# Optimization experiments

Measured on AMD Instinct MI355X. Metric: run time of the kernel, lower is better.

The kernel has to match this reference:

```python
import jax, jax.numpy as jnp
import numpy as np

B = 16384      # number of batched 6-node FC graphs
A = 6          # num_agents (nodes per graph)
D_OBS = 128    # raw observation dim
D_EMB = 250    # embedding / GAT feature dim
H = 3          # GAT heads (head outputs averaged to keep dim 250)
HID = 256
N_ACT = 5
NEG_SLOPE = 0.2


def setup_inputs() -> dict:
    key = jax.random.key(0)
    ks = jax.random.split(key, 16)
    def w(i, shape, scale=0.05):
        return jax.random.normal(ks[i], shape, dtype=jnp.float32) * scale
    return {
        "x": jax.random.normal(ks[0], (B * A, D_OBS), dtype=jnp.float32),
        "W_emb": w(1, (D_OBS, D_EMB)), "b_emb": jnp.zeros((D_EMB,), jnp.float32),
        "W_gat": w(2, (H, D_EMB, D_EMB)),
        "a_l": w(3, (H, D_EMB)), "a_r": w(4, (H, D_EMB)),
        "W1": w(5, (2 * D_EMB, HID)), "b1": jnp.zeros((HID,), jnp.float32),
        "W2": w(6, (HID, N_ACT)), "b2": jnp.zeros((N_ACT,), jnp.float32),
        "V1": w(7, (2 * D_EMB, HID)), "vb1": jnp.zeros((HID,), jnp.float32),
        "V2": w(8, (HID, 1)), "vb2": jnp.zeros((1,), jnp.float32),
    }


def reference(x, W_emb, b_emb, W_gat, a_l, a_r, W1, b1, W2, b2, V1, vb1, V2, vb2):
    # embedding layer
    h = jax.nn.relu(x @ W_emb + b_emb)                       # [N, 250]
    hb = h.reshape(B, A, D_EMB)                              # [B, 6, 250]
    # GAT on fully-connected 6-node graphs (incl. self edges), dense-masked form
    Wh = jnp.einsum("bad,hde->bhae", hb, W_gat)              # [B, H, 6, 250]
    el = jnp.einsum("bhae,he->bha", Wh, a_l)                 # dst term
    er = jnp.einsum("bhae,he->bha", Wh, a_r)                 # src term
    e = jax.nn.leaky_relu(el[:, :, :, None] + er[:, :, None, :], NEG_SLOPE)  # [B,H,6,6]
    attn = jax.nn.softmax(e, axis=-1)                        # edge softmax over neighbors
    gat = jnp.einsum("bhij,bhje->bhie", attn, Wh).mean(axis=1)  # mean over heads -> [B,6,250]
    feat = jnp.concatenate([hb, gat], axis=-1).reshape(B * A, 2 * D_EMB)  # [N, 500]
    # actor head (reg1)
    probs = jax.nn.softmax(jax.nn.relu(feat @ W1 + b1) @ W2 + b2, axis=-1)  # [N, 5]
    # critic head (reg2)
    value = jax.nn.relu(feat @ V1 + vb1) @ V2 + vb2           # [N, 1]
    return jnp.concatenate([probs, value], axis=-1)          # [N, 6]
```

## Files before the change

kernel.cpp:

```cpp
#include <hip/hip_runtime.h>

typedef unsigned short u16;
typedef unsigned int   u32;
typedef unsigned long long u64;
typedef __attribute__((ext_vector_type(4))) int   i32x4;
typedef __attribute__((ext_vector_type(4))) float f32x4;
typedef __attribute__((ext_vector_type(8))) short s16x8;

#define NROWS 98304L
#define LDF   512

__device__ __forceinline__ u16 f2bf(float x) {
  union { float f; u32 u; } v; v.f = x;
  return (u16)((v.u + 0x7FFFu + ((v.u >> 16) & 1u)) >> 16);
}
__device__ __forceinline__ float bf2f(u16 b) {
  union { float f; u32 u; } v; v.u = ((u32)b) << 16;
  return v.f;
}

__device__ __forceinline__ void gload_lds16(const u16* g, u16* l) {
  __builtin_amdgcn_global_load_lds(
      (const __attribute__((address_space(1))) unsigned int*)g,
      (__attribute__((address_space(3))) unsigned int*)l, 16, 0, 0);
}

__global__ __launch_bounds__(256)
void prep_weights(const float* __restrict__ W_emb, const float* __restrict__ b_emb,
                  const float* __restrict__ W_gat, const float* __restrict__ a_l,
                  const float* __restrict__ a_r, const float* __restrict__ W1,
                  const float* __restrict__ b1, const float* __restrict__ V1,
                  const float* __restrict__ vb1,
                  u16* __restrict__ Wemb_t, u16* __restrict__ Wgat_t,
                  u16* __restrict__ W1V1_t, float* __restrict__ bembp,
                  float* __restrict__ b1vb1)
{
  const int idx = blockIdx.x * 256 + threadIdx.x;
  const int stride = gridDim.x * 256;
  for (int t = idx; t < 256 * 128; t += stride) {
    int n = t >> 7, k = t & 127;
    Wemb_t[t] = f2bf(n < 250 ? W_emb[k * 250 + n] : 0.f);
  }
  for (int t = idx; t < 3 * 256 * 256; t += stride) {
    int h = t >> 16, rem = t & 65535, e = rem >> 8, d = rem & 255;
    float v = 0.f;
    if (e < 250 && d < 250) {
      v = W_gat[(h * 250 + d) * 250 + e];
    } else if ((e == 250 || e == 251) && d < 250) {
      const float* av = ((e == 250) ? a_l : a_r) + h * 250;
      const float* wrow = W_gat + ((long)h * 250 + d) * 250;
      float s = 0.f;
      for (int q = 0; q < 250; q++) s += wrow[q] * av[q];
      v = s;
    }
    Wgat_t[t] = f2bf(v);
  }
  for (int t = idx; t < 512 * 512; t += stride) {
    int n = t >> 9, k = t & 511;
    const float* src = (n < 256) ? W1 : V1;
    int col = n & 255;
    float v = 0.f;
    if (k < 250) v = src[k * 256 + col];
    else if (k >= 256 && k < 506) v = src[(k - 6) * 256 + col];
    W1V1_t[t] = f2bf(v);
  }
  for (int t = idx; t < 512; t += stride) b1vb1[t] = (t < 256) ? b1[t] : vb1[t - 256];
  for (int t = idx; t < 256; t += stride) bembp[t] = (t < 250) ? b_emb[t] : 0.f;
}

__global__ __launch_bounds__(256)
void cvt_x(const float* __restrict__ x, u16* __restrict__ xb)
{
  const long n = NROWS * 128;
  long i = ((long)blockIdx.x * 256 + threadIdx.x) * 8;
  const long stride = (long)gridDim.x * 256 * 8;
  for (; i < n; i += stride) {
    f32x4 a = *(const f32x4*)(x + i);
    f32x4 b = *(const f32x4*)(x + i + 4);
    i32x4 o;
    o[0] = (int)((u32)f2bf(a[0]) | ((u32)f2bf(a[1]) << 16));
    o[1] = (int)((u32)f2bf(a[2]) | ((u32)f2bf(a[3]) << 16));
    o[2] = (int)((u32)f2bf(b[0]) | ((u32)f2bf(b[1]) << 16));
    o[3] = (int)((u32)f2bf(b[2]) | ((u32)f2bf(b[3]) << 16));
    *(i32x4*)(xb + i) = o;
  }
}

template<int KSTEPS, int EPI>
__global__ __launch_bounds__(256, 2)
void gemm_bf16(const u16* __restrict__ A, int lda,
               const u16* __restrict__ B, int ldb, long strideB,
               u16* __restrict__ C, int ldc, long strideC,
               const float* __restrict__ bias, int nb)
{
  __shared__ __align__(16) u16 At[128 * 64];
  __shared__ __align__(16) u16 Bt[128 * 64];
  const int tid = threadIdx.x;
  const int w = tid >> 6, lane = tid & 63;
  const int fl = lane & 15, fh = lane >> 4;
  const int wr = (w >> 1) * 64, wc = (w & 1) * 64;
  const int srow = lane >> 3;
  const int scol = (((lane & 7) ^ srow) << 3);
  const int swz = (fl & 7) << 3;

  const int nidx = blockIdx.x % nb;
  const int zidx = blockIdx.x / nb;
  const int midx = blockIdx.y;

  const u16* Ab = A + (long)midx * 128 * lda;
  const u16* Bb = B + (long)zidx * strideB + (long)nidx * 128 * ldb;
  u16* Cb = C + (long)zidx * strideC + (long)midx * 128 * ldc + nidx * 128;
  const float* biasb = bias + nidx * 128;

  f32x4 acc[4][4];
  #pragma unroll
  for (int m = 0; m < 4; m++)
    #pragma unroll
    for (int n = 0; n < 4; n++)
      acc[m][n] = f32x4{0.f, 0.f, 0.f, 0.f};

  for (int ks = 0; ks < KSTEPS; ks++) {
    __syncthreads();
    #pragma unroll
    for (int c = 0; c < 4; c++) {
      const int row = w * 32 + c * 8 + srow;
      gload_lds16(Ab + (long)row * lda + ks * 64 + scol, At + (w * 4 + c) * 512);
      gload_lds16(Bb + (long)row * ldb + ks * 64 + scol, Bt + (w * 4 + c) * 512);
    }
    __syncthreads();
    #pragma unroll
    for (int kk = 0; kk < 2; kk++) {
      s16x8 af[4], bfr[4];
      #pragma unroll
      for (int m = 0; m < 4; m++)
        af[m] = *(const s16x8*)(At + (wr + m * 16 + fl) * 64 + ((kk * 32 + fh * 8) ^ swz));
      #pragma unroll
      for (int n = 0; n < 4; n++)
        bfr[n] = *(const s16x8*)(Bt + (wc + n * 16 + fl) * 64 + ((kk * 32 + fh * 8) ^ swz));
      #pragma unroll
      for (int m = 0; m < 4; m++)
        #pragma unroll
        for (int n = 0; n < 4; n++)
          acc[m][n] = __builtin_amdgcn_mfma_f32_16x16x32_bf16(af[m], bfr[n], acc[m][n], 0, 0, 0);
    }
  }
  #pragma unroll
  for (int m = 0; m < 4; m++) {
    const int r0 = wr + m * 16 + fh * 4;
    #pragma unroll
    for (int n = 0; n < 4; n++) {
      const int col = wc + n * 16 + fl;
      float bvv = 0.f;
      if constexpr (EPI == 1) bvv = biasb[col];
      f32x4 v = acc[m][n];
      #pragma unroll
      for (int r = 0; r < 4; r++) {
        float xv = v[r];
        if constexpr (EPI == 1) xv = fmaxf(xv + bvv, 0.f);
        Cb[(long)(r0 + r) * ldc + col] = f2bf(xv);
      }
    }
  }
}

__global__ __launch_bounds__(1024, 2)
void gemm3_heads(const u16* __restrict__ A,
                 const u16* __restrict__ B,
                 const float* __restrict__ b1vb1,
                 const float* __restrict__ W2,
                 const float* __restrict__ b2,
                 const float* __restrict__ V2,
                 const float* __restrict__ vb2,
                 float* __restrict__ out)
{
  __shared__ __align__(16) u16 At[128 * 64];
  __shared__ __align__(16) u16 Bt[512 * 64];
  __shared__ float pstage[8][128][6];
  const int tid = threadIdx.x;
  const int w = tid >> 6, lane = tid & 63;
  const int fl = lane & 15, fh = lane >> 4;
  const int wrow = w >> 3, wcol = w & 7;
  const int srow = lane >> 3;
  const int schunk = (((lane & 7) ^ srow) << 3);
  const int swz = (fl & 7) << 3;

  const u16* Ab = A + (long)blockIdx.x * 128 * 512;

  f32x4 acc[4][4];
  #pragma unroll
  for (int m = 0; m < 4; m++)
    #pragma unroll
    for (int n = 0; n < 4; n++)
      acc[m][n] = f32x4{0.f, 0.f, 0.f, 0.f};

  for (int ks = 0; ks < 8; ks++) {
    __syncthreads();
    gload_lds16(Ab + (long)(w * 8 + srow) * 512 + ks * 64 + schunk, At + w * 512);
    #pragma unroll
    for (int p = 0; p < 4; p++)
      gload_lds16(B + (long)(p * 128 + w * 8 + srow) * 512 + ks * 64 + schunk,
                  Bt + p * 8192 + w * 512);
    __syncthreads();
    #pragma unroll
    for (int kk = 0; kk < 2; kk++) {
      s16x8 af[4], bfr[4];
      #pragma unroll
      for (int m = 0; m < 4; m++)
        af[m] = *(const s16x8*)(At + (wrow * 64 + m * 16 + fl) * 64 + ((kk * 32 + fh * 8) ^ swz));
      #pragma unroll
      for (int n = 0; n < 4; n++)
        bfr[n] = *(const s16x8*)(Bt + (wcol * 64 + n * 16 + fl) * 64 + ((kk * 32 + fh * 8) ^ swz));
      #pragma unroll
      for (int m = 0; m < 4; m++)
        #pragma unroll
        for (int n = 0; n < 4; n++)
          acc[m][n] = __builtin_amdgcn_mfma_f32_16x16x32_bf16(af[m], bfr[n], acc[m][n], 0, 0, 0);
    }
  }

  float bv[4];
  #pragma unroll
  for (int n = 0; n < 4; n++) bv[n] = b1vb1[wcol * 64 + n * 16 + fl];

  if (wcol < 4) {
    #pragma unroll
    for (int m = 0; m < 4; m++) {
      float ps[4][5];
      #pragma unroll
      for (int r = 0; r < 4; r++)
        #pragma unroll
        for (int j = 0; j < 5; j++) ps[r][j] = 0.f;
      #pragma unroll
      for (int n = 0; n < 4; n++) {
        const int col = wcol * 64 + n * 16 + fl;
        const float* w2c = W2 + col * 5;
        float w2r[5];
        #pragma unroll
        for (int j = 0; j < 5; j++) w2r[j] = w2c[j];
        #pragma unroll
        for (int r = 0; r < 4; r++) {
          float hid = fmaxf(acc[m][n][r] + bv[n], 0.f);
          #pragma unroll
          for (int j = 0; j < 5; j++) ps[r][j] += hid * w2r[j];
        }
      }
      #pragma unroll
      for (int off = 1; off < 16; off <<= 1)
        #pragma unroll
        for (int r = 0; r < 4; r++)
          #pragma unroll
          for (int j = 0; j < 5; j++) ps[r][j] += __shfl_xor(ps[r][j], off, 16);
      if (fl == 0) {
        const int row = wrow * 64 + m * 16 + fh * 4;
        #pragma unroll
        for (int r = 0; r < 4; r++)
          #pragma unroll
          for (int j = 0; j < 5; j++) pstage[wcol][row + r][j] = ps[r][j];
      }
    }
  } else {
    #pragma unroll
    for (int m = 0; m < 4; m++) {
      float ps[4];
      #pragma unroll
      for (int r = 0; r < 4; r++) ps[r] = 0.f;
      #pragma unroll
      for (int n = 0; n < 4; n++) {
        const int col = wcol * 64 + n * 16 + fl;
        const float v2c = V2[col - 256];
        #pragma unroll
        for (int r = 0; r < 4; r++) {
          float hid = fmaxf(acc[m][n][r] + bv[n], 0.f);
          ps[r] += hid * v2c;
        }
      }
      #pragma unroll
      for (int off = 1; off < 16; off <<= 1)
        #pragma unroll
        for (int r = 0; r < 4; r++) ps[r] += __shfl_xor(ps[r], off, 16);
      if (fl == 0) {
        const int row = wrow * 64 + m * 16 + fh * 4;
        #pragma unroll
        for (int r = 0; r < 4; r++) pstage[wcol][row + r][5] = ps[r];
      }
    }
  }
  __syncthreads();

  if (tid < 128) {
    float lg[5];
    #pragma unroll
    for (int j = 0; j < 5; j++)
      lg[j] = pstage[0][tid][j] + pstage[1][tid][j] + pstage[2][tid][j] +
              pstage[3][tid][j] + b2[j];
    float val = pstage[4][tid][5] + pstage[5][tid][5] + pstage[6][tid][5] +
                pstage[7][tid][5] + vb2[0];
    float mx = -1e30f;
    #pragma unroll
    for (int j = 0; j < 5; j++) mx = fmaxf(mx, lg[j]);
    float s = 0.f, e[5];
    #pragma unroll
    for (int j = 0; j < 5; j++) { e[j] = __expf(lg[j] - mx); s += e[j]; }
    float inv = 1.f / s;
    float* op = out + ((long)blockIdx.x * 128 + tid) * 6;
    #pragma unroll
    for (int j = 0; j < 5; j++) op[j] = e[j] * inv;
    op[5] = val;
  }
}

__global__ __launch_bounds__(256)
void attn_gat(const u16* __restrict__ Wh, u16* __restrict__ feat)
{
  const int w = threadIdx.x >> 6, lane = threadIdx.x & 63;
  const long g = (long)blockIdx.x * 4 + w;
  const int c0 = lane * 4;

  u64 raw[3][6];
  #pragma unroll
  for (int h = 0; h < 3; h++)
    #pragma unroll
    for (int i = 0; i < 6; i++)
      raw[h][i] = *(const u64*)(Wh + (((long)h * NROWS + g * 6 + i) << 8) + c0);

  float gacc[6][4];
  #pragma unroll
  for (int i = 0; i < 6; i++)
    #pragma unroll
    for (int q = 0; q < 4; q++) gacc[i][q] = 0.f;

  #pragma unroll
  for (int h = 0; h < 3; h++) {
    float whf[6][4];
    #pragma unroll
    for (int i = 0; i < 6; i++) {
      u64 v = raw[h][i];
      whf[i][0] = bf2f((u16)v);
      whf[i][1] = bf2f((u16)(v >> 16));
      whf[i][2] = bf2f((u16)(v >> 32));
      whf[i][3] = bf2f((u16)(v >> 48));
    }
    float el[6], er[6];
    #pragma unroll
    for (int i = 0; i < 6; i++) {
      el[i] = __shfl(whf[i][2], 62, 64);
      er[i] = __shfl(whf[i][3], 62, 64);
    }
    #pragma unroll
    for (int i = 0; i < 6; i++) {
      float e[6]; float mx = -1e30f;
      #pragma unroll
      for (int j = 0; j < 6; j++) {
        float t = el[i] + er[j];
        t = (t > 0.f) ? t : 0.2f * t;
        e[j] = t; mx = fmaxf(mx, t);
      }
      float s = 0.f;
      #pragma unroll
      for (int j = 0; j < 6; j++) { e[j] = __expf(e[j] - mx); s += e[j]; }
      float inv = 1.f / s;
      #pragma unroll
      for (int j = 0; j < 6; j++) {
        float a = e[j] * inv;
        #pragma unroll
        for (int q = 0; q < 4; q++) gacc[i][q] += a * whf[j][q];
      }
    }
  }
  #pragma unroll
  for (int i = 0; i < 6; i++) {
    const float k = 1.f / 3.f;
    u64 o = (u64)f2bf(gacc[i][0] * k)
          | ((u64)f2bf(gacc[i][1] * k) << 16)
          | ((u64)f2bf(gacc[i][2] * k) << 32)
          | ((u64)f2bf(gacc[i][3] * k) << 48);
    *(u64*)(feat + (g * 6 + i) * LDF + 256 + c0) = o;
  }
}

extern "C" void kernel_launch(void* const* d_in, const int* in_sizes, int n_in,
                              void* d_out, int out_size, void* d_ws, size_t ws_size,
                              hipStream_t stream)
{
  const float* x     = (const float*)d_in[0];
  const float* W_emb = (const float*)d_in[1];
  const float* b_emb = (const float*)d_in[2];
  const float* W_gat = (const float*)d_in[3];
  const float* a_l   = (const float*)d_in[4];
  const float* a_r   = (const float*)d_in[5];
  const float* W1    = (const float*)d_in[6];
  const float* b1    = (const float*)d_in[7];
  const float* W2    = (const float*)d_in[8];
  const float* b2    = (const float*)d_in[9];
  const float* V1    = (const float*)d_in[10];
  const float* vb1   = (const float*)d_in[11];
  const float* V2    = (const float*)d_in[12];
  const float* vb2   = (const float*)d_in[13];

  char* ws = (char*)d_ws;
  u16* feat = (u16*)ws;
  char* r2  = ws + 100663296L;
  u16* xb   = (u16*)r2;
  u16* Whb  = (u16*)r2;
  char* wt  = r2 + 150994944L;
  u16*   Wemb_t = (u16*)wt;
  u16*   Wgat_t = (u16*)(wt + 65536);
  u16*   W1V1_t = (u16*)(wt + 458752);
  float* b1vb1  = (float*)(wt + 983040);
  float* bembp  = (float*)(wt + 985088);

  prep_weights<<<256, 256, 0, stream>>>(W_emb, b_emb, W_gat, a_l, a_r, W1, b1, V1, vb1,
                                        Wemb_t, Wgat_t, W1V1_t, bembp, b1vb1);
  cvt_x<<<2048, 256, 0, stream>>>(x, xb);
  gemm_bf16<2, 1><<<dim3(2, 768), 256, 0, stream>>>(xb, 128, Wemb_t, 128, 0L,
                                                    feat, 512, 0L, bembp, 2);
  gemm_bf16<4, 0><<<dim3(6, 768), 256, 0, stream>>>(feat, 512, Wgat_t, 256, 65536L,
                                                    Whb, 256, 25165824L, bembp, 2);
  attn_gat<<<4096, 256, 0, stream>>>(Whb, feat);
  gemm3_heads<<<768, 1024, 0, stream>>>(feat, W1V1_t, b1vb1, W2, b2, V2, vb2,
                                        (float*)d_out);
}
```

Measured before the change: 364.4 us.

## Fuse x fp32-to-bf16 conversion into embedding GEMM; split head GEMM into tiles

Removes the separate cvt_x pass: the embedding GEMM now reads fp32 x directly, converts it to bf16 in registers and writes it into swizzled LDS. The old 1024-thread head GEMM, which loaded all 512 weight columns per block, is replaced by a 256-thread kernel tiled over 4 column blocks. Each tile writes partial logits and values to a global scratch buffer, and a small final kernel sums them and applies the softmax. This saves a full read and write of x and should raise occupancy in the head GEMM. The cost is one extra launch, an extra round trip of the partials through memory, and A tiles that are reloaded for each column block.

```diff
diff --git a/kernel.cpp b/kernel.cpp
--- a/kernel.cpp
+++ b/kernel.cpp
@@ -68,30 +68,91 @@
   for (int t = idx; t < 256; t += stride) bembp[t] = (t < 250) ? b_emb[t] : 0.f;
 }
 
-__global__ __launch_bounds__(256)
-void cvt_x(const float* __restrict__ x, u16* __restrict__ xb)
-{
-  const long n = NROWS * 128;
-  long i = ((long)blockIdx.x * 256 + threadIdx.x) * 8;
-  const long stride = (long)gridDim.x * 256 * 8;
-  for (; i < n; i += stride) {
-    f32x4 a = *(const f32x4*)(x + i);
-    f32x4 b = *(const f32x4*)(x + i + 4);
-    i32x4 o;
-    o[0] = (int)((u32)f2bf(a[0]) | ((u32)f2bf(a[1]) << 16));
-    o[1] = (int)((u32)f2bf(a[2]) | ((u32)f2bf(a[3]) << 16));
-    o[2] = (int)((u32)f2bf(b[0]) | ((u32)f2bf(b[1]) << 16));
-    o[3] = (int)((u32)f2bf(b[2]) | ((u32)f2bf(b[3]) << 16));
-    *(i32x4*)(xb + i) = o;
-  }
-}
-
-template<int KSTEPS, int EPI>
+__global__ __launch_bounds__(256, 2)
+void gemm1f(const float* __restrict__ X,
+            const u16* __restrict__ B,
+            u16* __restrict__ C,
+            const float* __restrict__ bias)
+{
+  __shared__ __align__(16) u16 At[128 * 64];
+  __shared__ __align__(16) u16 Bt[128 * 64];
+  const int tid = threadIdx.x;
+  const int w = tid >> 6, lane = tid & 63;
+  const int fl = lane & 15, fh = lane >> 4;
+  const int wr = (w >> 1) * 64, wc = (w & 1) * 64;
+  const int srow = lane >> 3;
+  const int slot = lane & 7;
+  const int schunk = ((slot ^ srow) << 3);
+  const int swz = (fl & 7) << 3;
+
+  const int nidx = blockIdx.x;
+  const int midx = blockIdx.y;
+
+  const float* Ax = X + (long)midx * 128 * 128;
+  const u16* Bb = B + nidx * 128 * 128;
+  u16* Cb = C + (long)midx * 128 * LDF + nidx * 128;
+  const float* biasb = bias + nidx * 128;
+
+  f32x4 acc[4][4];
+  #pragma unroll
+  for (int m = 0; m < 4; m++)
+    #pragma unroll
+    for (int n = 0; n < 4; n++)
+      acc[m][n] = f32x4{0.f, 0.f, 0.f, 0.f};
+
+  for (int ks = 0; ks < 2; ks++) {
+    __syncthreads();
+    #pragma unroll
+    for (int c = 0; c < 4; c++) {
+      const int row = w * 32 + c * 8 + srow;
+      gload_lds16(Bb + (long)row * 128 + ks * 64 + schunk, Bt + (w * 4 + c) * 512);
+      const float* src = Ax + (long)row * 128 + ks * 64 + schunk;
+      f32x4 lo = *(const f32x4*)src;
+      f32x4 hi = *(const f32x4*)(src + 4);
+      i32x4 o;
+      o[0] = (int)((u32)f2bf(lo[0]) | ((u32)f2bf(lo[1]) << 16));
+      o[1] = (int)((u32)f2bf(lo[2]) | ((u32)f2bf(lo[3]) << 16));
+      o[2] = (int)((u32)f2bf(hi[0]) | ((u32)f2bf(hi[1]) << 16));
+      o[3] = (int)((u32)f2bf(hi[2]) | ((u32)f2bf(hi[3]) << 16));
+      *(i32x4*)(At + row * 64 + slot * 8) = o;
+    }
+    __syncthreads();
+    #pragma unroll
+    for (int kk = 0; kk < 2; kk++) {
+      s16x8 af[4], bfr[4];
+      #pragma unroll
+      for (int m = 0; m < 4; m++)
+        af[m] = *(const s16x8*)(At + (wr + m * 16 + fl) * 64 + ((kk * 32 + fh * 8) ^ swz));
+      #pragma unroll
+      for (int n = 0; n < 4; n++)
+        bfr[n] = *(const s16x8*)(Bt + (wc + n * 16 + fl) * 64 + ((kk * 32 + fh * 8) ^ swz));
+      #pragma unroll
+      for (int m = 0; m < 4; m++)
+        #pragma unroll
+        for (int n = 0; n < 4; n++)
+          acc[m][n] = __builtin_amdgcn_mfma_f32_16x16x32_bf16(af[m], bfr[n], acc[m][n], 0, 0, 0);
+    }
+  }
+  #pragma unroll
+  for (int m = 0; m < 4; m++) {
+    const int r0 = wr + m * 16 + fh * 4;
+    #pragma unroll
+    for (int n = 0; n < 4; n++) {
+      const int col = wc + n * 16 + fl;
+      const float bvv = biasb[col];
+      f32x4 v = acc[m][n];
+      #pragma unroll
+      for (int r = 0; r < 4; r++)
+        Cb[(long)(r0 + r) * LDF + col] = f2bf(fmaxf(v[r] + bvv, 0.f));
+    }
+  }
+}
+
+template<int KSTEPS>
 __global__ __launch_bounds__(256, 2)
 void gemm_bf16(const u16* __restrict__ A, int lda,
                const u16* __restrict__ B, int ldb, long strideB,
-               u16* __restrict__ C, int ldc, long strideC,
-               const float* __restrict__ bias, int nb)
+               u16* __restrict__ C, int ldc, long strideC, int nb)
 {
   __shared__ __align__(16) u16 At[128 * 64];
   __shared__ __align__(16) u16 Bt[128 * 64];
@@ -110,7 +171,6 @@
   const u16* Ab = A + (long)midx * 128 * lda;
   const u16* Bb = B + (long)zidx * strideB + (long)nidx * 128 * ldb;
   u16* Cb = C + (long)zidx * strideC + (long)midx * 128 * ldc + nidx * 128;
-  const float* biasb = bias + nidx * 128;
 
   f32x4 acc[4][4];
   #pragma unroll
@@ -150,41 +210,39 @@
     #pragma unroll
     for (int n = 0; n < 4; n++) {
       const int col = wc + n * 16 + fl;
-      float bvv = 0.f;
-      if constexpr (EPI == 1) bvv = biasb[col];
       f32x4 v = acc[m][n];
       #pragma unroll
-      for (int r = 0; r < 4; r++) {
-        float xv = v[r];
-        if constexpr (EPI == 1) xv = fmaxf(xv + bvv, 0.f);
-        Cb[(long)(r0 + r) * ldc + col] = f2bf(xv);
-      }
-    }
-  }
-}
-
-__global__ __launch_bounds__(1024, 2)
-void gemm3_heads(const u16* __restrict__ A,
-                 const u16* __restrict__ B,
-                 const float* __restrict__ b1vb1,
-                 const float* __restrict__ W2,
-                 const float* __restrict__ b2,
-                 const float* __restrict__ V2,
-                 const float* __restrict__ vb2,
-                 float* __restrict__ out)
+      for (int r = 0; r < 4; r++)
+        Cb[(long)(r0 + r) * ldc + col] = f2bf(v[r]);
+    }
+  }
+}
+
+__global__ __launch_bounds__(256, 2)
+void gemm3p(const u16* __restrict__ A,
+            const u16* __restrict__ B,
+            const float* __restrict__ b1vb1,
+            const float* __restrict__ W2,
+            const float* __restrict__ V2,
+            float* __restrict__ partials)
 {
   __shared__ __align__(16) u16 At[128 * 64];
-  __shared__ __align__(16) u16 Bt[512 * 64];
-  __shared__ float pstage[8][128][6];
+  __shared__ __align__(16) u16 Bt[128 * 64];
+  __shared__ float pstage[2][128][6];
   const int tid = threadIdx.x;
   const int w = tid >> 6, lane = tid & 63;
   const int fl = lane & 15, fh = lane >> 4;
-  const int wrow = w >> 3, wcol = w & 7;
+  const int wr = (w >> 1) * 64, wc = (w & 1) * 64;
+  const int wcid = w & 1;
   const int srow = lane >> 3;
-  const int schunk = (((lane & 7) ^ srow) << 3);
+  const int scol = (((lane & 7) ^ srow) << 3);
   const int swz = (fl & 7) << 3;
 
-  const u16* Ab = A + (long)blockIdx.x * 128 * 512;
+  const int nidx = blockIdx.x;
+  const int midx = blockIdx.y;
+
+  const u16* Ab = A + (long)midx * 128 * 512;
+  const u16* Bb = B + (long)nidx * 128 * 512;
 
   f32x4 acc[4][4];
   #pragma unroll
@@ -195,21 +253,22 @@
 
   for (int ks = 0; ks < 8; ks++) {
     __syncthreads();
-    gload_lds16(Ab + (long)(w * 8 + srow) * 512 + ks * 64 + schunk, At + w * 512);
-    #pragma unroll
-    for (int p = 0; p < 4; p++)
-      gload_lds16(B + (long)(p * 128 + w * 8 + srow) * 512 + ks * 64 + schunk,
-                  Bt + p * 8192 + w * 512);
+    #pragma unroll
+    for (int c = 0; c < 4; c++) {
+      const int row = w * 32 + c * 8 + srow;
+      gload_lds16(Ab + (long)row * 512 + ks * 64 + scol, At + (w * 4 + c) * 512);
+      gload_lds16(Bb + (long)row * 512 + ks * 64 + scol, Bt + (w * 4 + c) * 512);
+    }
     __syncthreads();
     #pragma unroll
     for (int kk = 0; kk < 2; kk++) {
       s16x8 af[4], bfr[4];
       #pragma unroll
       for (int m = 0; m < 4; m++)
-        af[m] = *(const s16x8*)(At + (wrow * 64 + m * 16 + fl) * 64 + ((kk * 32 + fh * 8) ^ swz));
+        af[m] = *(const s16x8*)(At + (wr + m * 16 + fl) * 64 + ((kk * 32 + fh * 8) ^ swz));
       #pragma unroll
       for (int n = 0; n < 4; n++)
-        bfr[n] = *(const s16x8*)(Bt + (wcol * 64 + n * 16 + fl) * 64 + ((kk * 32 + fh * 8) ^ swz));
+        bfr[n] = *(const s16x8*)(Bt + (wc + n * 16 + fl) * 64 + ((kk * 32 + fh * 8) ^ swz));
       #pragma unroll
       for (int m = 0; m < 4; m++)
         #pragma unroll
@@ -220,9 +279,9 @@
 
   float bv[4];
   #pragma unroll
-  for (int n = 0; n < 4; n++) bv[n] = b1vb1[wcol * 64 + n * 16 + fl];
-
-  if (wcol < 4) {
+  for (int n = 0; n < 4; n++) bv[n] = b1vb1[nidx * 128 + wc + n * 16 + fl];
+
+  if (nidx < 2) {
     #pragma unroll
     for (int m = 0; m < 4; m++) {
       float ps[4][5];
@@ -232,11 +291,10 @@
         for (int j = 0; j < 5; j++) ps[r][j] = 0.f;
       #pragma unroll
       for (int n = 0; n < 4; n++) {
-        const int col = wcol * 64 + n * 16 + fl;
-        const float* w2c = W2 + col * 5;
+        const int gcol = nidx * 128 + wc + n * 16 + fl;
         float w2r[5];
         #pragma unroll
-        for (int j = 0; j < 5; j++) w2r[j] = w2c[j];
+        for (int j = 0; j < 5; j++) w2r[j] = W2[gcol * 5 + j];
         #pragma unroll
         for (int r = 0; r < 4; r++) {
           float hid = fmaxf(acc[m][n][r] + bv[n], 0.f);
@@ -251,11 +309,11 @@
           #pragma unroll
           for (int j = 0; j < 5; j++) ps[r][j] += __shfl_xor(ps[r][j], off, 16);
       if (fl == 0) {
-        const int row = wrow * 64 + m * 16 + fh * 4;
+        const int row = wr + m * 16 + fh * 4;
         #pragma unroll
         for (int r = 0; r < 4; r++)
           #pragma unroll
-          for (int j = 0; j < 5; j++) pstage[wcol][row + r][j] = ps[r][j];
+          for (int j = 0; j < 5; j++) pstage[wcid][row + r][j] = ps[r][j];
       }
     }
   } else {
@@ -266,47 +324,59 @@
       for (int r = 0; r < 4; r++) ps[r] = 0.f;
       #pragma unroll
       for (int n = 0; n < 4; n++) {
-        const int col = wcol * 64 + n * 16 + fl;
-        const float v2c = V2[col - 256];
-        #pragma unroll
-        for (int r = 0; r < 4; r++) {
-          float hid = fmaxf(acc[m][n][r] + bv[n], 0.f);
-          ps[r] += hid * v2c;
-        }
+        const int gcol = nidx * 128 + wc + n * 16 + fl - 256;
+        const float v2c = V2[gcol];
+        #pragma unroll
+        for (int r = 0; r < 4; r++)
+          ps[r] += fmaxf(acc[m][n][r] + bv[n], 0.f) * v2c;
       }
       #pragma unroll
       for (int off = 1; off < 16; off <<= 1)
         #pragma unroll
         for (int r = 0; r < 4; r++) ps[r] += __shfl_xor(ps[r], off, 16);
       if (fl == 0) {
-        const int row = wrow * 64 + m * 16 + fh * 4;
-        #pragma unroll
-        for (int r = 0; r < 4; r++) pstage[wcol][row + r][5] = ps[r];
+        const int row = wr + m * 16 + fh * 4;
+        #pragma unroll
+        for (int r = 0; r < 4; r++) pstage[wcid][row + r][5] = ps[r];
       }
     }
   }
   __syncthreads();
 
   if (tid < 128) {
-    float lg[5];
-    #pragma unroll
-    for (int j = 0; j < 5; j++)
-      lg[j] = pstage[0][tid][j] + pstage[1][tid][j] + pstage[2][tid][j] +
-              pstage[3][tid][j] + b2[j];
-    float val = pstage[4][tid][5] + pstage[5][tid][5] + pstage[6][tid][5] +
-                pstage[7][tid][5] + vb2[0];
-    float mx = -1e30f;
-    #pragma unroll
-    for (int j = 0; j < 5; j++) mx = fmaxf(mx, lg[j]);
-    float s = 0.f, e[5];
-    #pragma unroll
-    for (int j = 0; j < 5; j++) { e[j] = __expf(lg[j] - mx); s += e[j]; }
-    float inv = 1.f / s;
-    float* op = out + ((long)blockIdx.x * 128 + tid) * 6;
-    #pragma unroll
-    for (int j = 0; j < 5; j++) op[j] = e[j] * inv;
-    op[5] = val;
-  }
+    float* dst = partials + ((long)nidx * NROWS + (long)midx * 128 + tid) * 6;
+    if (nidx < 2) {
+      #pragma unroll
+      for (int j = 0; j < 5; j++)
+        dst[j] = pstage[0][tid][j] + pstage[1][tid][j];
+    } else {
+      dst[5] = pstage[0][tid][5] + pstage[1][tid][5];
+    }
+  }
+}
+
+__global__ __launch_bounds__(256)
+void heads_final(const float* __restrict__ partials, const float* __restrict__ b2,
+                 const float* __restrict__ vb2, float* __restrict__ out)
+{
+  const long row = (long)blockIdx.x * 256 + threadIdx.x;
+  const long slab = NROWS * 6;
+  const float* p = partials + row * 6;
+  float lg[5];
+  #pragma unroll
+  for (int j = 0; j < 5; j++) lg[j] = p[j] + p[slab + j] + b2[j];
+  const float val = p[2 * slab + 5] + p[3 * slab + 5] + vb2[0];
+  float mx = -1e30f;
+  #pragma unroll
+  for (int j = 0; j < 5; j++) mx = fmaxf(mx, lg[j]);
+  float s = 0.f, e[5];
+  #pragma unroll
+  for (int j = 0; j < 5; j++) { e[j] = __expf(lg[j] - mx); s += e[j]; }
+  const float inv = 1.f / s;
+  float* op = out + row * 6;
+  #pragma unroll
+  for (int j = 0; j < 5; j++) op[j] = e[j] * inv;
+  op[5] = val;
 }
 
 __global__ __launch_bounds__(256)
@@ -400,8 +470,8 @@
   char* ws = (char*)d_ws;
   u16* feat = (u16*)ws;
   char* r2  = ws + 100663296L;
-  u16* xb   = (u16*)r2;
-  u16* Whb  = (u16*)r2;
+  u16*   Whb      = (u16*)r2;
+  float* partials = (float*)r2;
   char* wt  = r2 + 150994944L;
   u16*   Wemb_t = (u16*)wt;
   u16*   Wgat_t = (u16*)(wt + 65536);
@@ -411,12 +481,10 @@
 
   prep_weights<<<256, 256, 0, stream>>>(W_emb, b_emb, W_gat, a_l, a_r, W1, b1, V1, vb1,
                                         Wemb_t, Wgat_t, W1V1_t, bembp, b1vb1);
-  cvt_x<<<2048, 256, 0, stream>>>(x, xb);
-  gemm_bf16<2, 1><<<dim3(2, 768), 256, 0, stream>>>(xb, 128, Wemb_t, 128, 0L,
-                                                    feat, 512, 0L, bembp, 2);
-  gemm_bf16<4, 0><<<dim3(6, 768), 256, 0, stream>>>(feat, 512, Wgat_t, 256, 65536L,
-                                                    Whb, 256, 25165824L, bembp, 2);
+  gemm1f<<<dim3(2, 768), 256, 0, stream>>>(x, Wemb_t, feat, bembp);
+  gemm_bf16<4><<<dim3(6, 768), 256, 0, stream>>>(feat, 512, Wgat_t, 256, 65536L,
+                                                 Whb, 256, 25165824L, 2);
   attn_gat<<<4096, 256, 0, stream>>>(Whb, feat);
-  gemm3_heads<<<768, 1024, 0, stream>>>(feat, W1V1_t, b1vb1, W2, b2, V2, vb2,
-                                        (float*)d_out);
-}
+  gemm3p<<<dim3(4, 768), 256, 0, stream>>>(feat, W1V1_t, b1vb1, W2, V2, partials);
+  heads_final<<<384, 256, 0, stream>>>(partials, b2, vb2, (float*)d_out);
+}
```

Result: no change. 364.4 us (+0.0%).
